# Kernel tuning notes

Hardware: AMD Instinct MI355X
Metric: run time of the kernel (lower is better)

## Reference

```python
import jax, jax.numpy as jnp
import numpy as np

B = 16384
OUT = 128          # output_size (per conditioning frame)
NCOND = 3
HID = 32           # MLP3 hidden
LSTM_H = 64        # lstm_output_size (input == hidden)
NPRED = 25
EPS = 1e-5


def setup_inputs() -> dict:
    key = jax.random.key(0)
    ks = jax.random.split(key, 20)
    d = {
        "x0": jax.random.normal(ks[0], (B, OUT), jnp.float32),
        "x1": jax.random.normal(ks[1], (B, OUT), jnp.float32),
        "x2": jax.random.normal(ks[2], (B, OUT), jnp.float32),
        # MLP3: Linear(384->32), BN, ReLU, Linear(32->32), BN, ReLU, Linear(32->64)
        "W1": jax.random.normal(ks[3], (HID, OUT * NCOND), jnp.float32) * 0.05,
        "b1": jnp.full((HID,), 0.03, jnp.float32),
        "g1": jnp.ones((HID,), jnp.float32),
        "beta1": jnp.zeros((HID,), jnp.float32),
        "W2": jax.random.normal(ks[4], (HID, HID), jnp.float32) * 0.1,
        "b2": jnp.full((HID,), 0.03, jnp.float32),
        "g2": jnp.ones((HID,), jnp.float32),
        "beta2": jnp.zeros((HID,), jnp.float32),
        "W3": jax.random.normal(ks[5], (LSTM_H, HID), jnp.float32) * 0.1,
        "b3": jnp.full((LSTM_H,), 0.03, jnp.float32),
        # LSTM (torch gate order i,f,g,o): weight_ih (4H,H), weight_hh (4H,H)
        "Wih": jax.random.normal(ks[6], (4 * LSTM_H, LSTM_H), jnp.float32) * 0.08,
        "Whh": jax.random.normal(ks[7], (4 * LSTM_H, LSTM_H), jnp.float32) * 0.08,
        "bih": jnp.zeros((4 * LSTM_H,), jnp.float32),
        "bhh": jnp.zeros((4 * LSTM_H,), jnp.float32),
    }
    return d


def _bn_train(h, g, b):
    # BatchNorm1d in training mode: biased batch statistics
    m = jnp.mean(h, axis=0)
    v = jnp.var(h, axis=0)
    return g * (h - m) * jax.lax.rsqrt(v + EPS) + b


def _lstm_step(inp, h, c, Wih, Whh, bih, bhh):
    gates = inp @ Wih.T + bih + h @ Whh.T + bhh  # (B, 4H)
    i, f, g, o = jnp.split(gates, 4, axis=1)
    c_new = jax.nn.sigmoid(f) * c + jax.nn.sigmoid(i) * jnp.tanh(g)
    h_new = jax.nn.sigmoid(o) * jnp.tanh(c_new)
    return h_new, c_new


def reference(x0, x1, x2, W1, b1, g1, beta1, W2, b2, g2, beta2, W3, b3,
              Wih, Whh, bih, bhh):
    x = jnp.concatenate([x0, x1, x2], axis=1)          # (B, 384)
    h = jax.nn.relu(_bn_train(x @ W1.T + b1, g1, beta1))
    h = jax.nn.relu(_bn_train(h @ W2.T + b2, g2, beta2))
    m = h @ W3.T + b3                                   # (B, 64)

    h0 = jnp.zeros((m.shape[0], LSTM_H), m.dtype)
    c0 = jnp.zeros_like(h0)
    # initial conditioning step (output discarded except as state/next input)
    h1, c1 = _lstm_step(m, h0, c0, Wih, Whh, bih, bhh)

    def step(carry, _):
        hh, cc = carry
        # loop feeds previous output back as input; output == h for 1-layer LSTM
        hn, cn = _lstm_step(hh, hh, cc, Wih, Whh, bih, bhh)
        return (hn, cn), hn

    _, outs = jax.lax.scan(step, (h1, c1), None, length=NPRED)  # (25, B, 64)
    return jnp.transpose(outs, (1, 0, 2))                        # (B, 25, 64)
```

## Files before the change

kernel.cpp:

```cpp
#include <hip/hip_runtime.h>


#define EPSV 1e-5f
#define LOG2E 1.4426950408889634f
#define K2    2.8853900817779268f

typedef __attribute__((ext_vector_type(8))) short bf16x8;
typedef __attribute__((ext_vector_type(4))) float f32x4;

__device__ __forceinline__ float rcp_f(float x) { return __builtin_amdgcn_rcpf(x); }
__device__ __forceinline__ void split_bf16(float x, ushort& hi, ushort& lo) {
    unsigned xb = __builtin_bit_cast(unsigned, x);
    hi = (ushort)(xb >> 16);
    float hif = __builtin_bit_cast(float, xb & 0xffff0000u);
    unsigned lb = __builtin_bit_cast(unsigned, x - hif);
    lo = (ushort)(lb >> 16);
}
__device__ __forceinline__ void split8(const float* w, bf16x8& hiv, bf16x8& lov) {
    ushort hs[8], ls[8];
    #pragma unroll
    for (int j = 0; j < 8; ++j) split_bf16(w[j], hs[j], ls[j]);
    hiv = *(bf16x8*)hs;
    lov = *(bf16x8*)ls;
}

__global__ __launch_bounds__(256) void k_red(
    const float* __restrict__ part, const float* __restrict__ g,
    const float* __restrict__ be, float* __restrict__ scsh,
    int do_prep,
    const float* __restrict__ Wih, const float* __restrict__ Whh,
    const float* __restrict__ bih, const float* __restrict__ bhh,
    ushort* __restrict__ Wih_hi, ushort* __restrict__ Wih_lo,
    ushort* __restrict__ Wsum_hi, ushort* __restrict__ Wsum_lo,
    float* __restrict__ bsum)
{
    __shared__ float rs[256], rq[256];
    const int ch = blockIdx.x, t = threadIdx.x;

    if (do_prep) {
        #pragma unroll
        for (int e = 0; e < 2; ++e) {
            int i = blockIdx.x * 512 + e * 256 + t;
            int j = i >> 6;
            float sc = (j >= 128 && j < 192) ? K2 : LOG2E;
            float wi  = Wih[i] * sc;
            float wsv = (Wih[i] + Whh[i]) * sc;
            ushort h, l;
            split_bf16(wi, h, l);  Wih_hi[i] = h;  Wih_lo[i] = l;
            split_bf16(wsv, h, l); Wsum_hi[i] = h; Wsum_lo[i] = l;
        }
        if (blockIdx.x == 0) {
            float sc = (t >= 128 && t < 192) ? K2 : LOG2E;
            bsum[t] = (bih[t] + bhh[t]) * sc;
        }
    }

    float s = (part[t * 32 + ch] + part[(t + 256) * 32 + ch]) +
              (part[(t + 512) * 32 + ch] + part[(t + 768) * 32 + ch]);
    float q = (part[32768 + t * 32 + ch] + part[32768 + (t + 256) * 32 + ch]) +
              (part[32768 + (t + 512) * 32 + ch] + part[32768 + (t + 768) * 32 + ch]);
    rs[t] = s; rq[t] = q;
    __syncthreads();
    #pragma unroll
    for (int off = 128; off > 0; off >>= 1) {
        if (t < off) { rs[t] += rs[t + off]; rq[t] += rq[t + off]; }
        __syncthreads();
    }
    if (t == 0) {
        float mu = rs[0] * (1.f / 16384.f);
        float va = rq[0] * (1.f / 16384.f) - mu * mu;
        float sc = g[ch] * rsqrtf(va + EPSV);
        scsh[ch] = sc; scsh[32 + ch] = be[ch] - mu * sc;
    }
}

__global__ __launch_bounds__(256, 2) void k_mlp1(
    const float* __restrict__ x0, const float* __restrict__ x1, const float* __restrict__ x2,
    const float* __restrict__ W1, const float* __restrict__ b1,
    float* __restrict__ pre, float* __restrict__ st1p)
{
    __shared__ __align__(16) ushort xhi[32 * 392];
    __shared__ __align__(16) ushort xlo[32 * 392];
    const int tid = threadIdx.x;
    const int r0  = blockIdx.x * 32;
    const int lane = tid & 63, l15 = lane & 15, lg = lane >> 4, q = tid >> 6;
    const int m0 = (q & 1) * 16, n0 = (q >> 1) * 16;

    bf16x8 WH[12], WL[12];
    {
        const float* wsrc = W1 + (size_t)(n0 + l15) * 384 + lg * 8;
        #pragma unroll
        for (int kt = 0; kt < 12; ++kt) {
            float w[8];
            float4 wa = *(const float4*)(wsrc + kt * 32);
            float4 wb = *(const float4*)(wsrc + kt * 32 + 4);
            w[0] = wa.x; w[1] = wa.y; w[2] = wa.z; w[3] = wa.w;
            w[4] = wb.x; w[5] = wb.y; w[6] = wb.z; w[7] = wb.w;
            split8(w, WH[kt], WL[kt]);
        }
    }

    for (int a = 0; a < 3; ++a) {
        const float* xp = (a == 0) ? x0 : (a == 1) ? x1 : x2;
        const float4* src = (const float4*)(xp + (size_t)r0 * 128);
        #pragma unroll
        for (int it = 0; it < 4; ++it) {
            int i = it * 256 + tid;
            int row = i >> 5, c4 = i & 31;
            float4 v = src[i];
            ushort h0, l0, h1, l1, h2, l2, h3, l3;
            split_bf16(v.x, h0, l0); split_bf16(v.y, h1, l1);
            split_bf16(v.z, h2, l2); split_bf16(v.w, h3, l3);
            int ofs = row * 392 + a * 128 + c4 * 4;
            *(ushort4*)&xhi[ofs] = make_ushort4(h0, h1, h2, h3);
            *(ushort4*)&xlo[ofs] = make_ushort4(l0, l1, l2, l3);
        }
    }
    __syncthreads();

    const float bias = b1[n0 + l15];
    f32x4 acc = {bias, bias, bias, bias};
    #pragma unroll
    for (int kt = 0; kt < 12; ++kt) {
        bf16x8 ahi = *(const bf16x8*)&xhi[(m0 + l15) * 392 + kt * 32 + lg * 8];
        bf16x8 alo = *(const bf16x8*)&xlo[(m0 + l15) * 392 + kt * 32 + lg * 8];
        acc = __builtin_amdgcn_mfma_f32_16x16x32_bf16(ahi, WH[kt], acc, 0, 0, 0);
        acc = __builtin_amdgcn_mfma_f32_16x16x32_bf16(ahi, WL[kt], acc, 0, 0, 0);
        acc = __builtin_amdgcn_mfma_f32_16x16x32_bf16(alo, WH[kt], acc, 0, 0, 0);
    }
    #pragma unroll
    for (int rg = 0; rg < 4; ++rg)
        pre[(size_t)(r0 + m0 + lg * 4 + rg) * 32 + n0 + l15] = acc[rg];
    float s  = (acc[0] + acc[1]) + (acc[2] + acc[3]);
    float sq = (acc[0] * acc[0] + acc[1] * acc[1]) + (acc[2] * acc[2] + acc[3] * acc[3]);
    s  += __shfl_xor(s, 16);  s  += __shfl_xor(s, 32);
    sq += __shfl_xor(sq, 16); sq += __shfl_xor(sq, 32);
    if (lg == 0) {
        int slot = (blockIdx.x * 2 + (q & 1)) * 32 + n0 + l15;
        st1p[slot] = s;
        st1p[32768 + slot] = sq;
    }
}

__global__ __launch_bounds__(256) void k_mlp2(
    float* __restrict__ pre, const float* __restrict__ scsh1,
    const float* __restrict__ W2, const float* __restrict__ b2,
    float* __restrict__ st2p)
{
    __shared__ __align__(16) ushort hhi[32 * 40];
    __shared__ __align__(16) ushort hlo[32 * 40];
    __shared__ float bnsc[32], bnsh[32];
    const int tid = threadIdx.x;
    const int r0  = blockIdx.x * 32;
    const int lane = tid & 63, l15 = lane & 15, lg = lane >> 4, q = tid >> 6;
    const int m0 = (q & 1) * 16, n0 = (q >> 1) * 16;

    bf16x8 W2H, W2L;
    {
        const float* wsrc = W2 + (size_t)(n0 + l15) * 32 + lg * 8;
        float w[8];
        float4 wa = *(const float4*)(wsrc);
        float4 wb = *(const float4*)(wsrc + 4);
        w[0] = wa.x; w[1] = wa.y; w[2] = wa.z; w[3] = wa.w;
        w[4] = wb.x; w[5] = wb.y; w[6] = wb.z; w[7] = wb.w;
        split8(w, W2H, W2L);
    }

    if (tid < 32) { bnsc[tid] = scsh1[tid]; bnsh[tid] = scsh1[32 + tid]; }
    __syncthreads();
    {
        int row = tid >> 3, c4 = tid & 7;
        float4 v = ((const float4*)(pre + (size_t)r0 * 32))[tid];
        float e0 = fmaxf(fmaf(v.x, bnsc[c4 * 4 + 0], bnsh[c4 * 4 + 0]), 0.f);
        float e1 = fmaxf(fmaf(v.y, bnsc[c4 * 4 + 1], bnsh[c4 * 4 + 1]), 0.f);
        float e2 = fmaxf(fmaf(v.z, bnsc[c4 * 4 + 2], bnsh[c4 * 4 + 2]), 0.f);
        float e3 = fmaxf(fmaf(v.w, bnsc[c4 * 4 + 3], bnsh[c4 * 4 + 3]), 0.f);
        ushort h0, l0, h1, l1, h2, l2, h3, l3;
        split_bf16(e0, h0, l0); split_bf16(e1, h1, l1);
        split_bf16(e2, h2, l2); split_bf16(e3, h3, l3);
        int ofs = row * 40 + c4 * 4;
        *(ushort4*)&hhi[ofs] = make_ushort4(h0, h1, h2, h3);
        *(ushort4*)&hlo[ofs] = make_ushort4(l0, l1, l2, l3);
    }
    __syncthreads();

    const float bias = b2[n0 + l15];
    f32x4 acc = {bias, bias, bias, bias};
    bf16x8 ahi = *(const bf16x8*)&hhi[(m0 + l15) * 40 + lg * 8];
    bf16x8 alo = *(const bf16x8*)&hlo[(m0 + l15) * 40 + lg * 8];
    acc = __builtin_amdgcn_mfma_f32_16x16x32_bf16(ahi, W2H, acc, 0, 0, 0);
    acc = __builtin_amdgcn_mfma_f32_16x16x32_bf16(ahi, W2L, acc, 0, 0, 0);
    acc = __builtin_amdgcn_mfma_f32_16x16x32_bf16(alo, W2H, acc, 0, 0, 0);

    #pragma unroll
    for (int rg = 0; rg < 4; ++rg)
        pre[(size_t)(r0 + m0 + lg * 4 + rg) * 32 + n0 + l15] = acc[rg];
    float s  = (acc[0] + acc[1]) + (acc[2] + acc[3]);
    float sq = (acc[0] * acc[0] + acc[1] * acc[1]) + (acc[2] * acc[2] + acc[3] * acc[3]);
    s  += __shfl_xor(s, 16);  s  += __shfl_xor(s, 32);
    sq += __shfl_xor(sq, 16); sq += __shfl_xor(sq, 32);
    if (lg == 0) {
        int slot = (blockIdx.x * 2 + (q & 1)) * 32 + n0 + l15;
        st2p[slot] = s;
        st2p[32768 + slot] = sq;
    }
}

__global__ __launch_bounds__(256, 2) void k_lstm(
    const float* __restrict__ pre, const float* __restrict__ scsh2,
    const float* __restrict__ W3, const float* __restrict__ b3,
    const ushort* __restrict__ Wih_hi, const ushort* __restrict__ Wih_lo,
    const ushort* __restrict__ Wsum_hi, const ushort* __restrict__ Wsum_lo,
    const float* __restrict__ bsum, float* __restrict__ out)
{
    __shared__ __align__(16) ushort hhi[2][2][16][72];
    __shared__ __align__(16) ushort hlo[2][2][16][72];
    __shared__ float bn2sc[32], bn2sh[32];
    const int tid  = threadIdx.x;
    const int lane = tid & 63, l15 = lane & 15, lg = lane >> 4, q = tid >> 6;
    const int r0   = blockIdx.x * 32;

    if (tid < 32) { bn2sc[tid] = scsh2[tid]; bn2sh[tid] = scsh2[32 + tid]; }
    __syncthreads();

    {
        const int row = tid & 31, seg = tid >> 5;
        float h2[32];
        const float4* pr = (const float4*)(pre + (size_t)(r0 + row) * 32);
        #pragma unroll
        for (int j4 = 0; j4 < 8; ++j4) {
            float4 v = pr[j4];
            h2[j4 * 4 + 0] = v.x; h2[j4 * 4 + 1] = v.y;
            h2[j4 * 4 + 2] = v.z; h2[j4 * 4 + 3] = v.w;
        }
        #pragma unroll
        for (int j = 0; j < 32; ++j) h2[j] = fmaxf(fmaf(h2[j], bn2sc[j], bn2sh[j]), 0.f);
        #pragma unroll
        for (int uu = 0; uu < 8; ++uu) {
            int u = seg * 8 + uu;
            const float* w = W3 + u * 32;
            float a0 = 0.f, a1 = 0.f, a2 = 0.f, a3 = 0.f;
            #pragma unroll
            for (int k = 0; k < 32; k += 4) {
                a0 = fmaf(h2[k + 0], w[k + 0], a0);
                a1 = fmaf(h2[k + 1], w[k + 1], a1);
                a2 = fmaf(h2[k + 2], w[k + 2], a2);
                a3 = fmaf(h2[k + 3], w[k + 3], a3);
            }
            float m = b3[u] + ((a0 + a1) + (a2 + a3));
            ushort mh, ml; split_bf16(m, mh, ml);
            hhi[row >> 4][0][row & 15][u] = mh;
            hlo[row >> 4][0][row & 15][u] = ml;
        }
    }

    float bias[4];
    #pragma unroll
    for (int nt = 0; nt < 4; ++nt) bias[nt] = bsum[nt * 64 + q * 16 + l15];
    float cA[4] = {0.f, 0.f, 0.f, 0.f}, cB[4] = {0.f, 0.f, 0.f, 0.f};

    float* obA[4];
    float* obB[4];
    #pragma unroll
    for (int rg = 0; rg < 4; ++rg) {
        obA[rg] = out + (size_t)(r0 + lg * 4 + rg) * 1600 + (q * 16 + l15);
        obB[rg] = out + (size_t)(r0 + 16 + lg * 4 + rg) * 1600 + (q * 16 + l15);
    }

    bf16x8 Bhi[4][2], Blo[4][2];
    const size_t wofs = (size_t)(q * 16 + l15) * 64 + lg * 8;
    #pragma unroll
    for (int nt = 0; nt < 4; ++nt)
        #pragma unroll
        for (int kt = 0; kt < 2; ++kt) {
            Bhi[nt][kt] = *(const bf16x8*)(Wih_hi + (size_t)nt * 4096 + wofs + kt * 32);
            Blo[nt][kt] = *(const bf16x8*)(Wih_lo + (size_t)nt * 4096 + wofs + kt * 32);
        }
    __syncthreads();

    if ((blockIdx.x >> 8) & 1) __builtin_amdgcn_s_sleep(46);

#define MFMA_GATES(ACC, G, BUF)                                                  \
    {                                                                            \
        _Pragma("unroll")                                                        \
        for (int nt = 0; nt < 4; ++nt)                                           \
            ACC[nt] = (f32x4){bias[nt], bias[nt], bias[nt], bias[nt]};           \
        _Pragma("unroll")                                                        \
        for (int kt = 0; kt < 2; ++kt) {                                         \
            bf16x8 ahi = *(const bf16x8*)&hhi[G][BUF][l15][kt * 32 + lg * 8];    \
            bf16x8 alo = *(const bf16x8*)&hlo[G][BUF][l15][kt * 32 + lg * 8];    \
            _Pragma("unroll")                                                    \
            for (int nt = 0; nt < 4; ++nt) {                                     \
                ACC[nt] = __builtin_amdgcn_mfma_f32_16x16x32_bf16(ahi, Bhi[nt][kt], ACC[nt], 0, 0, 0); \
                ACC[nt] = __builtin_amdgcn_mfma_f32_16x16x32_bf16(ahi, Blo[nt][kt], ACC[nt], 0, 0, 0); \
                ACC[nt] = __builtin_amdgcn_mfma_f32_16x16x32_bf16(alo, Bhi[nt][kt], ACC[nt], 0, 0, 0); \
            }                                                                    \
        }                                                                        \
    }

#define ACT(ACC, C, G, WBUF, OB, SLOT, WRST)                                     \
    {                                                                            \
        const int u = q * 16 + l15;                                              \
        _Pragma("unroll")                                                        \
        for (int rg = 0; rg < 4; ++rg) {                                         \
            int row = lg * 4 + rg;                                               \
            float iv = ACC[0][rg], fv = ACC[1][rg];                              \
            float gv = ACC[2][rg], ov = ACC[3][rg];                              \
            float Af = __builtin_amdgcn_exp2f(-fv);                              \
            float Ai = __builtin_amdgcn_exp2f(-iv);                              \
            float Bg = __builtin_amdgcn_exp2f(gv);                               \
            float sig = (Bg - 1.f) * rcp_f((1.f + Ai) * (Bg + 1.f));             \
            float cc = C[rg] * rcp_f(1.f + Af) + sig;                            \
            C[rg] = cc;                                                          \
            float Ao = __builtin_amdgcn_exp2f(-ov);                              \
            float C2 = __builtin_amdgcn_exp2f(cc * K2);                          \
            float hn = (C2 - 1.f) * rcp_f((1.f + Ao) * (C2 + 1.f));              \
            ushort hh, hl; split_bf16(hn, hh, hl);                               \
            hhi[G][WBUF][row][u] = hh;                                           \
            hlo[G][WBUF][row][u] = hl;                                           \
            if (WRST)                                                            \
                OB[rg][(size_t)(SLOT) * 64] = hn;                                \
        }                                                                        \
    }

    f32x4 accA[4], accB[4];

    MFMA_GATES(accA, 0, 0);
    MFMA_GATES(accB, 1, 0);
    #pragma unroll
    for (int nt = 0; nt < 4; ++nt)
        #pragma unroll
        for (int kt = 0; kt < 2; ++kt) {
            Bhi[nt][kt] = *(const bf16x8*)(Wsum_hi + (size_t)nt * 4096 + wofs + kt * 32);
            Blo[nt][kt] = *(const bf16x8*)(Wsum_lo + (size_t)nt * 4096 + wofs + kt * 32);
        }
    ACT(accA, cA, 0, 1, obA, 0, 0);
    ACT(accB, cB, 1, 1, obB, 0, 0);
    __syncthreads();

    #pragma unroll 1
    for (int s = 1; s <= 25; ++s) {
        const int rb = s & 1, wb = rb ^ 1;
        MFMA_GATES(accA, 0, rb);
        MFMA_GATES(accB, 1, rb);
        ACT(accA, cA, 0, wb, obA, s - 1, 1);
        ACT(accB, cB, 1, wb, obB, s - 1, 1);
        __syncthreads();
    }

#undef MFMA_GATES
#undef ACT
}

extern "C" void kernel_launch(void* const* d_in, const int* in_sizes, int n_in,
                              void* d_out, int out_size, void* d_ws, size_t ws_size,
                              hipStream_t stream) {
    const float* x0   = (const float*)d_in[0];
    const float* x1   = (const float*)d_in[1];
    const float* x2   = (const float*)d_in[2];
    const float* W1   = (const float*)d_in[3];
    const float* b1   = (const float*)d_in[4];
    const float* g1   = (const float*)d_in[5];
    const float* be1  = (const float*)d_in[6];
    const float* W2   = (const float*)d_in[7];
    const float* b2   = (const float*)d_in[8];
    const float* g2   = (const float*)d_in[9];
    const float* be2  = (const float*)d_in[10];
    const float* W3   = (const float*)d_in[11];
    const float* b3   = (const float*)d_in[12];
    const float* Wih  = (const float*)d_in[13];
    const float* Whh  = (const float*)d_in[14];
    const float* bih  = (const float*)d_in[15];
    const float* bhh  = (const float*)d_in[16];

    float* ws    = (float*)d_ws;
    float* pre   = ws;
    float* st1p  = ws + 524288;
    float* st2p  = ws + 589824;
    float* scsh1 = ws + 655360;
    float* scsh2 = ws + 655424;
    float* bsum  = ws + 655488;
    ushort* ub   = (ushort*)(ws + 655744);
    ushort* Wih_hi  = ub;
    ushort* Wih_lo  = ub + 16384;
    ushort* Wsum_hi = ub + 32768;
    ushort* Wsum_lo = ub + 49152;

    hipLaunchKernelGGL(k_mlp1, dim3(512), dim3(256), 0, stream,
                       x0, x1, x2, W1, b1, pre, st1p);
    hipLaunchKernelGGL(k_red, dim3(32), dim3(256), 0, stream,
                       st1p, g1, be1, scsh1,
                       1, Wih, Whh, bih, bhh, Wih_hi, Wih_lo, Wsum_hi, Wsum_lo, bsum);
    hipLaunchKernelGGL(k_mlp2, dim3(512), dim3(256), 0, stream,
                       pre, scsh1, W2, b2, st2p);
    hipLaunchKernelGGL(k_red, dim3(32), dim3(256), 0, stream,
                       st2p, g2, be2, scsh2,
                       0, Wih, Whh, bih, bhh, Wih_hi, Wih_lo, Wsum_hi, Wsum_lo, bsum);
    hipLaunchKernelGGL(k_lstm, dim3(512), dim3(256), 0, stream,
                       pre, scsh2, W3, b3,
                       Wih_hi, Wih_lo, Wsum_hi, Wsum_lo, bsum, (float*)d_out);
}
```

Measured before the change: 82.08 us.

## Split LSTM row groups across twice as many waves per block

The LSTM kernel now launches 512 threads per block, so each wave owns one 16-row group and one 16-unit slice instead of two row groups, halving per-wave serial MFMA and activation work and doubling wave-level parallelism. The staggered s_sleep for alternate blocks is removed. Separately, k_mlp2 reads the BN scale/shift directly from global as float4 instead of staging it in shared memory, dropping one barrier. The trade-off is higher register and occupancy pressure with 512-thread blocks at two blocks per CU, and each wave still holds its own copy of the weight fragments.

```diff
diff --git a/kernel.cpp b/kernel.cpp
--- a/kernel.cpp
+++ b/kernel.cpp
@@ -149,7 +149,6 @@
 {
     __shared__ __align__(16) ushort hhi[32 * 40];
     __shared__ __align__(16) ushort hlo[32 * 40];
-    __shared__ float bnsc[32], bnsh[32];
     const int tid = threadIdx.x;
     const int r0  = blockIdx.x * 32;
     const int lane = tid & 63, l15 = lane & 15, lg = lane >> 4, q = tid >> 6;
@@ -166,15 +165,15 @@
         split8(w, W2H, W2L);
     }
 
-    if (tid < 32) { bnsc[tid] = scsh1[tid]; bnsh[tid] = scsh1[32 + tid]; }
-    __syncthreads();
     {
         int row = tid >> 3, c4 = tid & 7;
+        float4 scv = *(const float4*)(scsh1 + c4 * 4);
+        float4 shv = *(const float4*)(scsh1 + 32 + c4 * 4);
         float4 v = ((const float4*)(pre + (size_t)r0 * 32))[tid];
-        float e0 = fmaxf(fmaf(v.x, bnsc[c4 * 4 + 0], bnsh[c4 * 4 + 0]), 0.f);
-        float e1 = fmaxf(fmaf(v.y, bnsc[c4 * 4 + 1], bnsh[c4 * 4 + 1]), 0.f);
-        float e2 = fmaxf(fmaf(v.z, bnsc[c4 * 4 + 2], bnsh[c4 * 4 + 2]), 0.f);
-        float e3 = fmaxf(fmaf(v.w, bnsc[c4 * 4 + 3], bnsh[c4 * 4 + 3]), 0.f);
+        float e0 = fmaxf(fmaf(v.x, scv.x, shv.x), 0.f);
+        float e1 = fmaxf(fmaf(v.y, scv.y, shv.y), 0.f);
+        float e2 = fmaxf(fmaf(v.z, scv.z, shv.z), 0.f);
+        float e3 = fmaxf(fmaf(v.w, scv.w, shv.w), 0.f);
         ushort h0, l0, h1, l1, h2, l2, h3, l3;
         split_bf16(e0, h0, l0); split_bf16(e1, h1, l1);
         split_bf16(e2, h2, l2); split_bf16(e3, h3, l3);
@@ -206,7 +205,7 @@
     }
 }
 
-__global__ __launch_bounds__(256, 2) void k_lstm(
+__global__ __launch_bounds__(512, 2) void k_lstm(
     const float* __restrict__ pre, const float* __restrict__ scsh2,
     const float* __restrict__ W3, const float* __restrict__ b3,
     const ushort* __restrict__ Wih_hi, const ushort* __restrict__ Wih_lo,
@@ -217,7 +216,8 @@
     __shared__ __align__(16) ushort hlo[2][2][16][72];
     __shared__ float bn2sc[32], bn2sh[32];
     const int tid  = threadIdx.x;
-    const int lane = tid & 63, l15 = lane & 15, lg = lane >> 4, q = tid >> 6;
+    const int lane = tid & 63, l15 = lane & 15, lg = lane >> 4;
+    const int w = tid >> 6, g = w & 1, qd = w >> 1;
     const int r0   = blockIdx.x * 32;
 
     if (tid < 32) { bn2sc[tid] = scsh2[tid]; bn2sh[tid] = scsh2[32 + tid]; }
@@ -236,16 +236,16 @@
         #pragma unroll
         for (int j = 0; j < 32; ++j) h2[j] = fmaxf(fmaf(h2[j], bn2sc[j], bn2sh[j]), 0.f);
         #pragma unroll
-        for (int uu = 0; uu < 8; ++uu) {
-            int u = seg * 8 + uu;
-            const float* w = W3 + u * 32;
+        for (int uu = 0; uu < 4; ++uu) {
+            int u = seg * 4 + uu;
+            const float* wp = W3 + u * 32;
             float a0 = 0.f, a1 = 0.f, a2 = 0.f, a3 = 0.f;
             #pragma unroll
             for (int k = 0; k < 32; k += 4) {
-                a0 = fmaf(h2[k + 0], w[k + 0], a0);
-                a1 = fmaf(h2[k + 1], w[k + 1], a1);
-                a2 = fmaf(h2[k + 2], w[k + 2], a2);
-                a3 = fmaf(h2[k + 3], w[k + 3], a3);
+                a0 = fmaf(h2[k + 0], wp[k + 0], a0);
+                a1 = fmaf(h2[k + 1], wp[k + 1], a1);
+                a2 = fmaf(h2[k + 2], wp[k + 2], a2);
+                a3 = fmaf(h2[k + 3], wp[k + 3], a3);
             }
             float m = b3[u] + ((a0 + a1) + (a2 + a3));
             ushort mh, ml; split_bf16(m, mh, ml);
@@ -256,19 +256,16 @@
 
     float bias[4];
     #pragma unroll
-    for (int nt = 0; nt < 4; ++nt) bias[nt] = bsum[nt * 64 + q * 16 + l15];
-    float cA[4] = {0.f, 0.f, 0.f, 0.f}, cB[4] = {0.f, 0.f, 0.f, 0.f};
-
-    float* obA[4];
-    float* obB[4];
-    #pragma unroll
-    for (int rg = 0; rg < 4; ++rg) {
-        obA[rg] = out + (size_t)(r0 + lg * 4 + rg) * 1600 + (q * 16 + l15);
-        obB[rg] = out + (size_t)(r0 + 16 + lg * 4 + rg) * 1600 + (q * 16 + l15);
-    }
+    for (int nt = 0; nt < 4; ++nt) bias[nt] = bsum[nt * 64 + qd * 16 + l15];
+    float c[4] = {0.f, 0.f, 0.f, 0.f};
+
+    float* ob[4];
+    #pragma unroll
+    for (int rg = 0; rg < 4; ++rg)
+        ob[rg] = out + (size_t)(r0 + g * 16 + lg * 4 + rg) * 1600 + (qd * 16 + l15);
 
     bf16x8 Bhi[4][2], Blo[4][2];
-    const size_t wofs = (size_t)(q * 16 + l15) * 64 + lg * 8;
+    const size_t wofs = (size_t)(qd * 16 + l15) * 64 + lg * 8;
     #pragma unroll
     for (int nt = 0; nt < 4; ++nt)
         #pragma unroll
@@ -278,17 +275,15 @@
         }
     __syncthreads();
 
-    if ((blockIdx.x >> 8) & 1) __builtin_amdgcn_s_sleep(46);
-
-#define MFMA_GATES(ACC, G, BUF)                                                  \
+#define MFMA_GATES(ACC, BUF)                                                     \
     {                                                                            \
         _Pragma("unroll")                                                        \
         for (int nt = 0; nt < 4; ++nt)                                           \
             ACC[nt] = (f32x4){bias[nt], bias[nt], bias[nt], bias[nt]};           \
         _Pragma("unroll")                                                        \
         for (int kt = 0; kt < 2; ++kt) {                                         \
-            bf16x8 ahi = *(const bf16x8*)&hhi[G][BUF][l15][kt * 32 + lg * 8];    \
-            bf16x8 alo = *(const bf16x8*)&hlo[G][BUF][l15][kt * 32 + lg * 8];    \
+            bf16x8 ahi = *(const bf16x8*)&hhi[g][BUF][l15][kt * 32 + lg * 8];    \
+            bf16x8 alo = *(const bf16x8*)&hlo[g][BUF][l15][kt * 32 + lg * 8];    \
             _Pragma("unroll")                                                    \
             for (int nt = 0; nt < 4; ++nt) {                                     \
                 ACC[nt] = __builtin_amdgcn_mfma_f32_16x16x32_bf16(ahi, Bhi[nt][kt], ACC[nt], 0, 0, 0); \
@@ -298,9 +293,9 @@
         }                                                                        \
     }
 
-#define ACT(ACC, C, G, WBUF, OB, SLOT, WRST)                                     \
+#define ACT(ACC, WBUF, SLOT, WRST)                                               \
     {                                                                            \
-        const int u = q * 16 + l15;                                              \
+        const int u = qd * 16 + l15;                                             \
         _Pragma("unroll")                                                        \
         for (int rg = 0; rg < 4; ++rg) {                                         \
             int row = lg * 4 + rg;                                               \
@@ -310,23 +305,22 @@
             float Ai = __builtin_amdgcn_exp2f(-iv);                              \
             float Bg = __builtin_amdgcn_exp2f(gv);                               \
             float sig = (Bg - 1.f) * rcp_f((1.f + Ai) * (Bg + 1.f));             \
-            float cc = C[rg] * rcp_f(1.f + Af) + sig;                            \
-            C[rg] = cc;                                                          \
+            float cc = c[rg] * rcp_f(1.f + Af) + sig;                            \
+            c[rg] = cc;                                                          \
             float Ao = __builtin_amdgcn_exp2f(-ov);                              \
             float C2 = __builtin_amdgcn_exp2f(cc * K2);                          \
             float hn = (C2 - 1.f) * rcp_f((1.f + Ao) * (C2 + 1.f));              \
             ushort hh, hl; split_bf16(hn, hh, hl);                               \
-            hhi[G][WBUF][row][u] = hh;                                           \
-            hlo[G][WBUF][row][u] = hl;                                           \
+            hhi[g][WBUF][row][u] = hh;                                           \
+            hlo[g][WBUF][row][u] = hl;                                           \
             if (WRST)                                                            \
-                OB[rg][(size_t)(SLOT) * 64] = hn;                                \
+                ob[rg][(size_t)(SLOT) * 64] = hn;                                \
         }                                                                        \
     }
 
-    f32x4 accA[4], accB[4];
-
-    MFMA_GATES(accA, 0, 0);
-    MFMA_GATES(accB, 1, 0);
+    f32x4 acc[4];
+
+    MFMA_GATES(acc, 0);
     #pragma unroll
     for (int nt = 0; nt < 4; ++nt)
         #pragma unroll
@@ -334,17 +328,14 @@
             Bhi[nt][kt] = *(const bf16x8*)(Wsum_hi + (size_t)nt * 4096 + wofs + kt * 32);
             Blo[nt][kt] = *(const bf16x8*)(Wsum_lo + (size_t)nt * 4096 + wofs + kt * 32);
         }
-    ACT(accA, cA, 0, 1, obA, 0, 0);
-    ACT(accB, cB, 1, 1, obB, 0, 0);
+    ACT(acc, 1, 0, 0);
     __syncthreads();
 
     #pragma unroll 1
     for (int s = 1; s <= 25; ++s) {
         const int rb = s & 1, wb = rb ^ 1;
-        MFMA_GATES(accA, 0, rb);
-        MFMA_GATES(accB, 1, rb);
-        ACT(accA, cA, 0, wb, obA, s - 1, 1);
-        ACT(accB, cB, 1, wb, obB, s - 1, 1);
+        MFMA_GATES(acc, rb);
+        ACT(acc, wb, s - 1, 1);
         __syncthreads();
     }
 
@@ -396,7 +387,7 @@
     hipLaunchKernelGGL(k_red, dim3(32), dim3(256), 0, stream,
                        st2p, g2, be2, scsh2,
                        0, Wih, Whh, bih, bhh, Wih_hi, Wih_lo, Wsum_hi, Wsum_lo, bsum);
-    hipLaunchKernelGGL(k_lstm, dim3(512), dim3(256), 0, stream,
+    hipLaunchKernelGGL(k_lstm, dim3(512), dim3(512), 0, stream,
                        pre, scsh2, W3, b3,
                        Wih_hi, Wih_lo, Wsum_hi, Wsum_lo, bsum, (float*)d_out);
 }
```

After: 84.19 us. 1.03x slower.
